# Kernel optimization log

Hardware: AMD Instinct MI355X
Metric: run time of the kernel (lower is better)

The kernel has to match this reference:

```python
import jax, jax.numpy as jnp
import numpy as np

EMSIZE = 2048
NCLASS = 128
D1 = 2
D2 = 2
NSENT = 32768


def setup_inputs() -> dict:
    key = jax.random.key(0)
    k1, k2, k3 = jax.random.split(key, 3)
    x = jax.random.normal(k1, (NSENT, 1, EMSIZE), dtype=jnp.float32)
    # Scaled-normal params (original uses nn.init.normal_; scaling keeps tanh unsaturated)
    W1 = jax.random.normal(k2, (D1 + 1, EMSIZE, NCLASS), dtype=jnp.float32) / np.float32(np.sqrt(EMSIZE))
    b1 = jnp.zeros((1, NCLASS), dtype=jnp.float32)
    W2 = jax.random.normal(k3, (D2 + 1, NCLASS, NCLASS), dtype=jnp.float32) / np.float32(np.sqrt(NCLASS))
    b2 = jnp.zeros((1, NCLASS), dtype=jnp.float32)
    return {"structural_representations": x, "W1": W1, "b1": b1, "W2": W2, "b2": b2}


def _shift_down(y, k, n):
    # y[p] -> y[p-k], zeros for p < k (causal shift along sentence axis)
    return jnp.pad(y, ((k, 0), (0, 0)))[:n] if k > 0 else y


def reference(structural_representations, W1, b1, W2, b2):
    x = structural_representations  # [N, 1, E]
    n, _, e = x.shape
    d1 = W1.shape[0] - 1
    d2 = W2.shape[0] - 1
    c = W1.shape[-1]
    xs = x.reshape(n, e)  # [N, E]

    # Stage 1: S[p] = sum_{k=0..d1, k<=p} (x[p-k] @ W1[k] + b1)
    Y = jnp.einsum('ne,kec->knc', xs, W1)  # [d1+1, N, C]: one big GEMM per tap
    S = sum(_shift_down(Y[k], k, n) for k in range(d1 + 1))  # windowed causal sum
    pos = jnp.arange(n)
    cnt1 = (jnp.minimum(pos, d1) + 1).astype(xs.dtype)  # bias added once per valid tap
    H = jnp.tanh(S + cnt1[:, None] * b1[0])  # [N, C]

    # Stage 2 (i >= d2): Z[i] = sum_{j=0..d2} H[i-d2+j] @ W2[j] + (d2+1)*b2
    G = jnp.einsum('nc,kcd->knd', H, W2)  # [d2+1, N, C]
    Z = sum(_shift_down(G[j], d2 - j, n) for j in range(d2 + 1)) + (d2 + 1) * b2[0]

    # Fallback for i < d2: single term tanh(x[i]@W1[0]+b1) @ W2[0] + b2
    H0 = jnp.tanh(xs @ W1[0] + b1[0])
    Z0 = H0 @ W2[0] + b2[0]
    Z = jnp.where((pos >= d2)[:, None], Z, Z0)

    out = jax.nn.log_softmax(Z, axis=-1)
    return out.reshape(n, 1, c)
```

## Files before the change

kernel.cpp:

```cpp
#include <hip/hip_runtime.h>
#include <math.h>

typedef __attribute__((ext_vector_type(8))) short short8;
typedef __attribute__((ext_vector_type(4))) float f32x4;

#define MFMA16(a, b, c) __builtin_amdgcn_mfma_f32_16x16x32_bf16((a), (b), (c), 0, 0, 0)

__device__ inline void gl_lds16(const void* g, void* l) {
  __builtin_amdgcn_global_load_lds(
      (const __attribute__((address_space(1))) void*)g,
      (__attribute__((address_space(3))) void*)l, 16, 0, 0);
}

__device__ inline unsigned int pack2(float lo, float hi) {
  unsigned int ulo = __float_as_uint(lo), uhi = __float_as_uint(hi);
  return (uhi & 0xFFFF0000u) | (ulo >> 16);
}
__device__ inline unsigned short f2bf_r(float f) {
  return (unsigned short)((__float_as_uint(f) + 0x8000u) >> 16);
}
__device__ inline float bf2f(unsigned short h) {
  return __uint_as_float(((unsigned int)h) << 16);
}

__global__ __launch_bounds__(256) void k_repack(const float* __restrict__ W1,
                                                const float* __restrict__ W2,
                                                unsigned short* __restrict__ W1bt,
                                                unsigned short* __restrict__ W2t) {
  __shared__ float tile[64 * 128];
  const int b = blockIdx.x, tid = threadIdx.x;
  if (b < 96) {
    const int k = b >> 5, et = b & 31;
    const int e0 = et * 64;
    const float* src = W1 + (size_t)k * 262144 + (size_t)e0 * 128;
#pragma unroll
    for (int i = 0; i < 8; ++i) {
      int idx4 = tid + i * 256;
      ((f32x4*)tile)[idx4] = ((const f32x4*)src)[idx4];
    }
    __syncthreads();
#pragma unroll
    for (int i = 0; i < 4; ++i) {
      int item = tid + i * 256;
      int c = item >> 3, eo = (item & 7) * 8;
      union { unsigned short h[8]; uint4 v; } t;
#pragma unroll
      for (int u = 0; u < 8; ++u) t.h[u] = f2bf_r(tile[(eo + u) * 128 + c]);
      *(uint4*)(W1bt + (size_t)(k * 128 + c) * 2048 + e0 + eo) = t.v;
    }
  } else {
    int idx = (b - 96) * 256 + tid;
    int j = idx >> 14, r = idx & 16383, d = r >> 7, c = r & 127;
    W2t[idx] = f2bf_r(W2[(size_t)j * 16384 + (size_t)c * 128 + d]);
  }
}

__global__ __launch_bounds__(512, 2) void k_fused(const float* __restrict__ X,
                                                  const unsigned short* __restrict__ Bt,
                                                  const unsigned short* __restrict__ W2t,
                                                  const float* __restrict__ b1,
                                                  const float* __restrict__ b2,
                                                  float* __restrict__ out) {
  constexpr int BUF = 43008, BOFF = 18432;
  __shared__ __align__(16) char smem[3 * 43008];
  unsigned short* Yt = (unsigned short*)smem;
  float* zbuf = (float*)(smem + 106624);

  const int r0 = blockIdx.x * 128;
  const int tid = threadIdx.x, wave = tid >> 6, lane = tid & 63;
  const int mrow = lane & 15, quad = lane >> 4;
  const int wr = wave >> 2, wc = wave & 3;

  const float* agp[3];
  {
    const int Ls[3] = { wave, wave + 8, 16 + wave };
#pragma unroll
    for (int jj = 0; jj < 3; ++jj) {
      int u = Ls[jj] * 64 + lane;
      int pl = u / 144, rr = u - pl * 144;
      if (pl > 7) pl = 7;
      int g = r0 - 4 + rr;
      if (g < 0) g = 0;
      if (g > 32767) g = 32767;
      agp[jj] = X + (size_t)g * 2048 + pl * 4;
    }
  }
  const unsigned short* bgp[3];
#pragma unroll
  for (int jj = 0; jj < 3; ++jj) {
    int col = (wave * 3 + jj) * 16 + (lane >> 2);
    int kc = (lane & 3) ^ ((lane >> 3) & 3);
    bgp[jj] = Bt + (size_t)col * 2048 + kc * 8;
  }

  f32x4 acc[5][6] = {};

  auto stage = [&](char* base) {
    gl_lds16(agp[0], base + wave * 1024);
    gl_lds16(agp[1], base + (wave + 8) * 1024);
    if (wave < 2) gl_lds16(agp[2], base + (16 + wave) * 1024);
#pragma unroll
    for (int jj = 0; jj < 3; ++jj)
      gl_lds16(bgp[jj], base + BOFF + (wave * 3 + jj) * 1024);
#pragma unroll
    for (int jj = 0; jj < 3; ++jj) agp[jj] += 32;
#pragma unroll
    for (int jj = 0; jj < 3; ++jj) bgp[jj] += 32;
  };

  auto compute = [&](const char* base) {
    const char* Ab = base;
    const unsigned short* Bb = (const unsigned short*)(base + BOFF);
    short8 af[5];
#pragma unroll
    for (int rt = 0; rt < 5; ++rt) {
      int row = wr * 80 + rt * 16 + mrow;
      f32x4 x0 = *(const f32x4*)(Ab + (quad * 2) * 2304 + row * 16);
      f32x4 x1 = *(const f32x4*)(Ab + (quad * 2 + 1) * 2304 + row * 16);
      union { unsigned int u[4]; short8 v; } tt;
      tt.u[0] = pack2(x0[0], x0[1]); tt.u[1] = pack2(x0[2], x0[3]);
      tt.u[2] = pack2(x1[0], x1[1]); tt.u[3] = pack2(x1[2], x1[3]);
      af[rt] = tt.v;
    }
#pragma unroll
    for (int ct = 0; ct < 6; ++ct) {
      int col = wc * 96 + ct * 16 + mrow;
      int slot = quad ^ ((mrow >> 1) & 3);
      short8 bf = *(const short8*)(Bb + col * 32 + slot * 8);
#pragma unroll
      for (int rt = 0; rt < 5; ++rt)
        acc[rt][ct] = MFMA16(af[rt], bf, acc[rt][ct]);
    }
  };

  stage(smem);
  stage(smem + BUF);

  int cur = 0, nx2 = 2;
  for (int t = 0; t < 63; ++t) {
    if (wave < 2) asm volatile("s_waitcnt vmcnt(6)" ::: "memory");
    else          asm volatile("s_waitcnt vmcnt(5)" ::: "memory");
    __builtin_amdgcn_s_barrier();
    __builtin_amdgcn_sched_barrier(0);
    if (t < 62) stage(smem + nx2 * BUF);
    compute(smem + cur * BUF);
    cur = (cur == 2) ? 0 : cur + 1;
    nx2 = (nx2 == 2) ? 0 : nx2 + 1;
  }
  asm volatile("s_waitcnt vmcnt(0)" ::: "memory");
  __builtin_amdgcn_s_barrier();
  __builtin_amdgcn_sched_barrier(0);
  compute(smem + cur * BUF);
  __syncthreads();

#pragma unroll
  for (int rt = 0; rt < 5; ++rt)
#pragma unroll
    for (int ct = 0; ct < 6; ++ct)
#pragma unroll
      for (int rg = 0; rg < 4; ++rg) {
        int l = wr * 80 + rt * 16 + quad * 4 + rg;
        int col = wc * 96 + ct * 16 + mrow;
        if (l < 136) Yt[l * 392 + col] = f2bf_r(acc[rt][ct][rg]);
      }
  __syncthreads();

  for (int idx = tid; idx < 130 * 128; idx += 512) {
    int hl = idx >> 7, c = idx & 127;
    int p = r0 - 2 + hl;
    int i = hl + 2;
    float h = 0.f;
    if (p >= 0) {
      float s = bf2f(Yt[i * 392 + c]);
      float cnt = 1.f;
      if (p >= 1) { s += bf2f(Yt[(i - 1) * 392 + 128 + c]); cnt += 1.f; }
      if (p >= 2) { s += bf2f(Yt[(i - 2) * 392 + 256 + c]); cnt += 1.f; }
      h = tanhf(fmaf(cnt, b1[c], s));
    }
    Yt[(i - 2) * 392 + 256 + c] = f2bf_r(h);
  }
  __syncthreads();

  f32x4 acc2[8] = {};
#pragma unroll
  for (int j = 0; j < 3; ++j) {
#pragma unroll
    for (int kk = 0; kk < 4; ++kk) {
      short8 a0 = *(const short8*)&Yt[(wave * 16 + mrow + j) * 392 + 256 + kk * 32 + quad * 8];
      const unsigned short* wp = W2t + (size_t)(j * 128 + mrow) * 128 + kk * 32 + quad * 8;
#pragma unroll
      for (int ct = 0; ct < 8; ++ct)
        acc2[ct] = MFMA16(a0, *(const short8*)(wp + ct * 16 * 128), acc2[ct]);
    }
  }

#pragma unroll
  for (int rg = 0; rg < 4; ++rg) {
    float z[8]; float m = -1e30f;
#pragma unroll
    for (int ct = 0; ct < 8; ++ct) {
      z[ct] = acc2[ct][rg] + 3.f * b2[ct * 16 + mrow];
      m = fmaxf(m, z[ct]);
    }
#pragma unroll
    for (int off = 1; off < 16; off <<= 1) m = fmaxf(m, __shfl_xor(m, off, 64));
    float s = 0.f;
#pragma unroll
    for (int ct = 0; ct < 8; ++ct) s += __expf(z[ct] - m);
#pragma unroll
    for (int off = 1; off < 16; off <<= 1) s += __shfl_xor(s, off, 64);
    float lse = m + __logf(s);
    int grow = r0 + wave * 16 + quad * 4 + rg;
    if (grow >= 2) {
      float* op = out + (size_t)grow * 128 + mrow;
#pragma unroll
      for (int ct = 0; ct < 8; ++ct) op[ct * 16] = z[ct] - lse;
    }
  }

  if (blockIdx.x == 0) {
    __syncthreads();
    int row = tid >> 7, d = tid & 127;
    if (tid < 256)
      zbuf[row * 128 + d] = tanhf(bf2f(Yt[(row + 4) * 392 + d]) + b1[d]);
    __syncthreads();
    float zv = 0.f;
    if (tid < 256) {
      zv = b2[d];
      for (int c = 0; c < 128; ++c)
        zv = fmaf(zbuf[row * 128 + c], bf2f(W2t[(size_t)d * 128 + c]), zv);
    }
    __syncthreads();
    if (tid < 256) zbuf[row * 128 + d] = zv;
    __syncthreads();
    if (tid < 256) {
      float m = -1e30f;
      for (int c = 0; c < 128; ++c) m = fmaxf(m, zbuf[row * 128 + c]);
      float s = 0.f;
      for (int c = 0; c < 128; ++c) s += __expf(zbuf[row * 128 + c] - m);
      out[(size_t)row * 128 + d] = zv - m - __logf(s);
    }
  }
}

extern "C" void kernel_launch(void* const* d_in, const int* in_sizes, int n_in,
                              void* d_out, int out_size, void* d_ws, size_t ws_size,
                              hipStream_t stream) {
  const float* X  = (const float*)d_in[0];
  const float* W1 = (const float*)d_in[1];
  const float* b1 = (const float*)d_in[2];
  const float* W2 = (const float*)d_in[3];
  const float* b2 = (const float*)d_in[4];
  float* out = (float*)d_out;

  unsigned short* W1bt = (unsigned short*)d_ws;
  unsigned short* W2t  = (unsigned short*)((char*)d_ws + 1572864);

  k_repack<<<288, 256, 0, stream>>>(W1, W2, W1bt, W2t);
  k_fused<<<256, 512, 0, stream>>>(X, W1bt, W2t, b1, b2, out);
}
```

Baseline: 441.6 us.

## Pre-pack X to bf16 tiled layout and use smaller-tile fused GEMM kernel

Adds a separate pass that converts X from fp32 to bf16 in a k-chunked, padded layout with zero halo rows, so the main kernel can stream A operands directly into LDS via global_load_lds instead of converting fp32 on the fly. The fused kernel is restructured to 64-row tiles with 256 threads, a double-buffered 32-wide K loop, and a 5x6 MFMA tile per wave covering the two halo rows. The old kernel is kept as a fallback when the workspace is too small. The cost is an extra full read of X plus a bf16 write and re-read, traded against cheaper, better-pipelined GEMM loads and more blocks.

New measurement: 492.6 us. 11.5% more time.

```diff
diff --git a/kernel.cpp b/kernel.cpp
--- a/kernel.cpp
+++ b/kernel.cpp
@@ -55,12 +55,208 @@
   }
 }
 
-__global__ __launch_bounds__(512, 2) void k_fused(const float* __restrict__ X,
-                                                  const unsigned short* __restrict__ Bt,
-                                                  const unsigned short* __restrict__ W2t,
-                                                  const float* __restrict__ b1,
-                                                  const float* __restrict__ b2,
-                                                  float* __restrict__ out) {
+__global__ __launch_bounds__(256) void k_xpack(const float* __restrict__ X,
+                                               unsigned short* __restrict__ Xbt) {
+  __shared__ float tile[64 * 256];
+  const int b = blockIdx.x, tid = threadIdx.x;
+  const int rbase = b * 64;
+  for (int kg = 0; kg < 8; ++kg) {
+    __syncthreads();
+#pragma unroll
+    for (int i = 0; i < 16; ++i) {
+      int item = tid + i * 256;
+      int row = item >> 6, c16 = item & 63;
+      f32x4 v = *(const f32x4*)(X + (size_t)(rbase + row) * 2048 + kg * 256 + c16 * 4);
+      int c0 = (c16 * 4) ^ ((row & 3) << 3);
+      *(f32x4*)&tile[row * 256 + c0] = v;
+    }
+    __syncthreads();
+#pragma unroll
+    for (int tc = 0; tc < 8; ++tc) {
+      int row2 = tid >> 2, c2 = (tid & 3) * 8;
+      int sw = (row2 & 3) << 3;
+      const float* p = &tile[row2 * 256 + ((tc * 32 + c2) ^ sw)];
+      f32x4 a = *(const f32x4*)p;
+      f32x4 bb = *(const f32x4*)(p + 4);
+      union { unsigned int u[4]; uint4 v; } t;
+      t.u[0] = pack2(a[0], a[1]);  t.u[1] = pack2(a[2], a[3]);
+      t.u[2] = pack2(bb[0], bb[1]); t.u[3] = pack2(bb[2], bb[3]);
+      *(uint4*)(Xbt + ((size_t)(kg * 8 + tc) * 32784 + rbase + 4 + row2) * 32 + c2) = t.v;
+    }
+  }
+  if (b == 0) {
+    for (int i = tid; i < 4096; i += 256) {
+      int t = i >> 6, rr = (i >> 4) & 3, c = (i & 15) * 2;
+      *(unsigned int*)(Xbt + ((size_t)t * 32784 + rr) * 32 + c) = 0u;
+    }
+  } else if (b == 511) {
+    for (int i = tid; i < 12288; i += 256) {
+      int t = i / 192, rem = i - t * 192;
+      int rr = 32772 + (rem >> 4), c = (rem & 15) * 2;
+      *(unsigned int*)(Xbt + ((size_t)t * 32784 + rr) * 32 + c) = 0u;
+    }
+  }
+}
+
+__global__ __launch_bounds__(256, 2) void k_fused_x(const unsigned short* __restrict__ Xbt,
+                                                    const unsigned short* __restrict__ Bt,
+                                                    const unsigned short* __restrict__ W2t,
+                                                    const float* __restrict__ b1,
+                                                    const float* __restrict__ b2,
+                                                    float* __restrict__ out) {
+  constexpr int BUF = 29696;
+  __shared__ __align__(16) char smem[63744];
+  unsigned short* Yt = (unsigned short*)smem;
+  float* zbuf = (float*)(smem + 62720);
+
+  const int r0 = blockIdx.x * 64;
+  const int tid = threadIdx.x, wave = tid >> 6, lane = tid & 63;
+  const int mrow = lane & 15, quad = lane >> 4;
+  const int srcsl = (lane & 3) ^ ((lane >> 3) & 3);
+
+  const unsigned short* axp[2];
+  axp[0] = Xbt + ((size_t)r0 + wave * 16 + (lane >> 2)) * 32 + srcsl * 8;
+  axp[1] = Xbt + ((size_t)r0 + 64 + (lane >> 2)) * 32 + srcsl * 8;
+  const unsigned short* bgp[6];
+#pragma unroll
+  for (int jj = 0; jj < 6; ++jj) {
+    int col = (wave * 6 + jj) * 16 + (lane >> 2);
+    bgp[jj] = Bt + (size_t)col * 2048 + srcsl * 8;
+  }
+
+  f32x4 acc[5][6] = {};
+
+  auto stage = [&](char* base) {
+    gl_lds16(axp[0], base + wave * 1024);
+    if (wave == 0) gl_lds16(axp[1], base + 4 * 1024);
+#pragma unroll
+    for (int jj = 0; jj < 6; ++jj)
+      gl_lds16(bgp[jj], base + 5120 + (wave * 6 + jj) * 1024);
+    axp[0] += (size_t)32784 * 32;
+    axp[1] += (size_t)32784 * 32;
+#pragma unroll
+    for (int jj = 0; jj < 6; ++jj) bgp[jj] += 32;
+  };
+
+  auto compute = [&](const char* base) {
+    const unsigned short* Ab = (const unsigned short*)base;
+    const unsigned short* Bb = (const unsigned short*)(base + 5120);
+    const int sl = (quad ^ ((mrow >> 1) & 3)) * 8;
+    short8 af[5];
+#pragma unroll
+    for (int rt = 0; rt < 5; ++rt)
+      af[rt] = *(const short8*)(Ab + (rt * 16 + mrow) * 32 + sl);
+#pragma unroll
+    for (int ct = 0; ct < 6; ++ct) {
+      int col = wave * 96 + ct * 16 + mrow;
+      short8 bf = *(const short8*)(Bb + col * 32 + sl);
+#pragma unroll
+      for (int rt = 0; rt < 5; ++rt)
+        acc[rt][ct] = MFMA16(af[rt], bf, acc[rt][ct]);
+    }
+  };
+
+  stage((char*)smem);
+#pragma unroll 2
+  for (int t = 0; t < 64; ++t) {
+    asm volatile("s_waitcnt vmcnt(0)" ::: "memory");
+    __builtin_amdgcn_s_barrier();
+    __builtin_amdgcn_sched_barrier(0);
+    if (t < 63) stage(smem + ((t + 1) & 1) * BUF);
+    compute(smem + (t & 1) * BUF);
+  }
+  __syncthreads();
+
+#pragma unroll
+  for (int rt = 0; rt < 5; ++rt)
+#pragma unroll
+    for (int ct = 0; ct < 6; ++ct)
+#pragma unroll
+      for (int rg = 0; rg < 4; ++rg) {
+        int l = rt * 16 + quad * 4 + rg;
+        int col = wave * 96 + ct * 16 + mrow;
+        Yt[l * 392 + col] = f2bf_r(acc[rt][ct][rg]);
+      }
+  __syncthreads();
+
+  for (int idx = tid; idx < 66 * 128; idx += 256) {
+    int hl = idx >> 7, c = idx & 127;
+    int p = r0 - 2 + hl;
+    int i = hl + 2;
+    float h = 0.f;
+    if (p >= 0) {
+      float s = bf2f(Yt[i * 392 + c]);
+      float cnt = 1.f;
+      if (p >= 1) { s += bf2f(Yt[(i - 1) * 392 + 128 + c]); cnt += 1.f; }
+      if (p >= 2) { s += bf2f(Yt[(i - 2) * 392 + 256 + c]); cnt += 1.f; }
+      h = tanhf(fmaf(cnt, b1[c], s));
+    }
+    Yt[(i - 2) * 392 + 256 + c] = f2bf_r(h);
+  }
+  __syncthreads();
+
+  f32x4 acc2[8] = {};
+#pragma unroll
+  for (int j = 0; j < 3; ++j) {
+#pragma unroll
+    for (int kk = 0; kk < 4; ++kk) {
+      short8 a0 = *(const short8*)&Yt[(wave * 16 + mrow + j) * 392 + 256 + kk * 32 + quad * 8];
+      const unsigned short* wp = W2t + (size_t)(j * 128 + mrow) * 128 + kk * 32 + quad * 8;
+#pragma unroll
+      for (int ct = 0; ct < 8; ++ct)
+        acc2[ct] = MFMA16(a0, *(const short8*)(wp + ct * 16 * 128), acc2[ct]);
+    }
+  }
+
+#pragma unroll
+  for (int rg = 0; rg < 4; ++rg) {
+    float z[8]; float m = -1e30f;
+#pragma unroll
+    for (int ct = 0; ct < 8; ++ct) {
+      z[ct] = acc2[ct][rg] + 3.f * b2[ct * 16 + mrow];
+      m = fmaxf(m, z[ct]);
+    }
+#pragma unroll
+    for (int off = 1; off < 16; off <<= 1) m = fmaxf(m, __shfl_xor(m, off, 64));
+    float s = 0.f;
+#pragma unroll
+    for (int ct = 0; ct < 8; ++ct) s += __expf(z[ct] - m);
+#pragma unroll
+    for (int off = 1; off < 16; off <<= 1) s += __shfl_xor(s, off, 64);
+    float lse = m + __logf(s);
+    int grow = r0 + wave * 16 + quad * 4 + rg;
+    if (grow >= 2) {
+      float* op = out + (size_t)grow * 128 + mrow;
+#pragma unroll
+      for (int ct = 0; ct < 8; ++ct) op[ct * 16] = z[ct] - lse;
+    }
+  }
+
+  if (blockIdx.x == 0) {
+    __syncthreads();
+    int row = tid >> 7, d = tid & 127;
+    zbuf[row * 128 + d] = tanhf(bf2f(Yt[(row + 4) * 392 + d]) + b1[d]);
+    __syncthreads();
+    float zv = b2[d];
+    for (int c = 0; c < 128; ++c)
+      zv = fmaf(zbuf[row * 128 + c], bf2f(W2t[(size_t)d * 128 + c]), zv);
+    __syncthreads();
+    zbuf[row * 128 + d] = zv;
+    __syncthreads();
+    float m = -1e30f;
+    for (int c = 0; c < 128; ++c) m = fmaxf(m, zbuf[row * 128 + c]);
+    float s = 0.f;
+    for (int c = 0; c < 128; ++c) s += __expf(zbuf[row * 128 + c] - m);
+    out[(size_t)row * 128 + d] = zv - m - __logf(s);
+  }
+}
+
+__global__ __launch_bounds__(512, 2) void k_fused_fb(const float* __restrict__ X,
+                                                     const unsigned short* __restrict__ Bt,
+                                                     const unsigned short* __restrict__ W2t,
+                                                     const float* __restrict__ b1,
+                                                     const float* __restrict__ b2,
+                                                     float* __restrict__ out) {
   constexpr int BUF = 43008, BOFF = 18432;
   __shared__ __align__(16) char smem[3 * 43008];
   unsigned short* Yt = (unsigned short*)smem;
@@ -255,7 +451,14 @@
 
   unsigned short* W1bt = (unsigned short*)d_ws;
   unsigned short* W2t  = (unsigned short*)((char*)d_ws + 1572864);
+  unsigned short* Xbt  = (unsigned short*)((char*)d_ws + 1703936);
+  const size_t need = 1703936 + (size_t)64 * 32784 * 64;
 
   k_repack<<<288, 256, 0, stream>>>(W1, W2, W1bt, W2t);
-  k_fused<<<256, 512, 0, stream>>>(X, W1bt, W2t, b1, b2, out);
-}
+  if (ws_size >= need) {
+    k_xpack<<<512, 256, 0, stream>>>(X, Xbt);
+    k_fused_x<<<512, 256, 0, stream>>>(Xbt, W1bt, W2t, b1, b2, out);
+  } else {
+    k_fused_fb<<<256, 512, 0, stream>>>(X, W1bt, W2t, b1, b2, out);
+  }
+}
```
